# Performance work log

Hardware: AMD Instinct MI355X
Metric: run time of the kernel (lower is better)

Reference implementation:

```python
import jax, jax.numpy as jnp
from jax import lax
import numpy as np

DIM = 512
HEADS = 8


def setup_inputs() -> dict:
    key = jax.random.key(0)
    k1, k2, k3, k4, k5 = jax.random.split(key, 5)
    B, C, H, W = 2, DIM, 64, 64
    x = jax.random.normal(k1, (B, C, H, W), dtype=jnp.float32)
    # depthwise 3x3 conv (groups=C, bias=False): torch OIHW with O=C, I=1
    dw_w = jax.random.normal(k2, (C, 1, 3, 3), dtype=jnp.float32) * (1.0 / 3.0)
    # 1x1 conv C -> 3C (bias=False)
    qkv_w = jax.random.normal(k3, (3 * C, C, 1, 1), dtype=jnp.float32) * (C ** -0.5)
    # 1x1 proj conv C -> C with bias
    proj_w = jax.random.normal(k4, (C, C, 1, 1), dtype=jnp.float32) * (C ** -0.5)
    proj_b = jax.random.normal(k5, (C,), dtype=jnp.float32) * 0.01
    return {"x": x, "dw_w": dw_w, "qkv_w": qkv_w, "proj_w": proj_w, "proj_b": proj_b}


def reference(x, dw_w, qkv_w, proj_w, proj_b):
    B, C, H, W = x.shape
    heads = HEADS
    dh = C // heads
    scale = dh ** -0.5
    N = H * W
    # depthwise 3x3, padding=1
    y = lax.conv_general_dilated(
        x, dw_w, window_strides=(1, 1), padding=((1, 1), (1, 1)),
        dimension_numbers=("NCHW", "OIHW", "NCHW"), feature_group_count=C)
    # 1x1 conv as matmul over channels -> (B, 3C, H, W)
    qkv = jnp.einsum("bchw,oc->bohw", y, qkv_w[:, :, 0, 0])
    # (B, 3, heads, dh, N) -> q,k,v each (B, heads, N, dh)
    qkv = qkv.reshape(B, 3, heads, dh, N).transpose(1, 0, 2, 4, 3)
    q, k, v = qkv[0], qkv[1], qkv[2]
    attn = jax.nn.softmax(jnp.einsum("bhnd,bhmd->bhnm", q, k) * scale, axis=-1)
    o = jnp.einsum("bhnm,bhmd->bhnd", attn, v)          # (B, heads, N, dh)
    o = o.transpose(0, 1, 3, 2).reshape(B, C, H, W)      # matches torch transpose(2,3).reshape
    out = jnp.einsum("bchw,oc->bohw", o, proj_w[:, :, 0, 0]) + proj_b[None, :, None, None]
    return out
```

## Files before the change

### kernel.cpp

```cpp
#include <hip/hip_runtime.h>
#include <hip/hip_bf16.h>

typedef __bf16 bf16_t;
typedef __bf16 bf16x4 __attribute__((ext_vector_type(4)));
typedef __bf16 bf16x8 __attribute__((ext_vector_type(8)));
typedef float f32x4 __attribute__((ext_vector_type(4)));
typedef float f32x8 __attribute__((ext_vector_type(8)));

#define MFMA16(a, b, c) __builtin_amdgcn_mfma_f32_16x16x32_bf16((a), (b), (c), 0, 0, 0)

#if __has_builtin(__builtin_amdgcn_exp2f)
#define EXP2(x) __builtin_amdgcn_exp2f(x)
#else
#define EXP2(x) exp2f(x)
#endif

#define AS1(p) ((const __attribute__((address_space(1))) void*)(p))
#define AS3(p) ((__attribute__((address_space(3))) void*)(p))

#define NPIX 4096
#define CDIM 512
#define QSCALE 0.1803368801111744f

#define KSTR 72
#define KTILE (64 * KSTR)

#define DWSTR 200

__device__ __forceinline__ bool detect_f32(const void* p) {
  const unsigned short* u = (const unsigned short*)p;
  int lane = threadIdx.x & 63;
  int f = 0;
#pragma unroll
  for (int j = 0; j < 4; ++j) {
    int e = (u[lane * 4 + j] >> 7) & 0xFF;
    f |= (e >= 138) ? 1 : 0;
  }
  return __ballot(f) != 0ull;
}

__global__ __launch_bounds__(256) void dwconv_kernel(
    const void* __restrict__ x_, const void* __restrict__ dww_,
    bf16_t* __restrict__ yt, const void* __restrict__ qkvw,
    const void* __restrict__ projw, bf16_t* __restrict__ wq,
    bf16_t* __restrict__ wp) {
  __shared__ bf16_t xs[64 * DWSTR];
  __shared__ float wsh[64 * 9];
  int bidx = blockIdx.x;
  int tid = threadIdx.x;

  if (bidx >= 1024) {
    int bid = bidx - 1024;
    const void* src;
    bf16_t* dst;
    int off;
    if (bid < 384) {
      src = qkvw; dst = wq; off = bid * 2048;
    } else {
      src = projw; dst = wp; off = (bid - 384) * 2048;
    }
    const bool wf32 = detect_f32(src);
    int i = off + tid * 8;
    if (wf32) {
      const float* p = (const float*)src + i;
      float4 t0 = *(const float4*)p;
      float4 t1 = *(const float4*)(p + 4);
      bf16x8 v;
      v[0] = (bf16_t)t0.x; v[1] = (bf16_t)t0.y;
      v[2] = (bf16_t)t0.z; v[3] = (bf16_t)t0.w;
      v[4] = (bf16_t)t1.x; v[5] = (bf16_t)t1.y;
      v[6] = (bf16_t)t1.z; v[7] = (bf16_t)t1.w;
      *(bf16x8*)&dst[i] = v;
    } else {
      *(bf16x8*)&dst[i] = *(const bf16x8*)((const bf16_t*)src + i);
    }
    return;
  }

  const bool f32m = detect_f32(x_);
  int c0 = (bidx & 7) << 6;
  int h = (bidx >> 3) & 63;
  int b = bidx >> 9;

  for (int i = tid; i < 576; i += 256)
    wsh[i] = f32m ? ((const float*)dww_)[c0 * 9 + i]
                  : (float)((const bf16_t*)dww_)[c0 * 9 + i];

  const size_t xoff = ((size_t)b * CDIM + c0) * NPIX;
#pragma unroll
  for (int r = 0; r < 3; ++r) {
    int hh = h + r - 1;
    bool ok = (unsigned)hh < 64u;
#pragma unroll
    for (int it = 0; it < 2; ++it) {
      int idx2 = tid + it * 256;
      int c = idx2 >> 3, ch = idx2 & 7;
      bf16x8 v = {};
      if (ok) {
        size_t gi = xoff + (size_t)c * NPIX + (size_t)hh * 64 + ch * 8;
        if (f32m) {
          const float* p = (const float*)x_ + gi;
          float4 t0 = *(const float4*)p;
          float4 t1 = *(const float4*)(p + 4);
          v[0] = (bf16_t)t0.x; v[1] = (bf16_t)t0.y;
          v[2] = (bf16_t)t0.z; v[3] = (bf16_t)t0.w;
          v[4] = (bf16_t)t1.x; v[5] = (bf16_t)t1.y;
          v[6] = (bf16_t)t1.z; v[7] = (bf16_t)t1.w;
        } else {
          v = *(const bf16x8*)((const bf16_t*)x_ + gi);
        }
      }
      *(bf16x8*)&xs[c * DWSTR + r * 64 + ch * 8] = v;
    }
  }
  __syncthreads();

  int c = tid & 63;
  int wb = tid >> 6;
  int w0 = wb * 16;
  float wreg[9];
#pragma unroll
  for (int j = 0; j < 9; ++j) wreg[j] = wsh[c * 9 + j];
  const bf16_t* xrow = &xs[c * DWSTR];

  float xw[3][18];
#pragma unroll
  for (int r = 0; r < 3; ++r) {
    bf16x8 v0 = *(const bf16x8*)&xrow[r * 64 + w0];
    bf16x8 v1 = *(const bf16x8*)&xrow[r * 64 + w0 + 8];
    xw[r][0] = (wb > 0) ? (float)xrow[r * 64 + w0 - 1] : 0.f;
    xw[r][17] = (wb < 3) ? (float)xrow[r * 64 + w0 + 16] : 0.f;
#pragma unroll
    for (int i = 0; i < 8; ++i) {
      xw[r][1 + i] = (float)v0[i];
      xw[r][9 + i] = (float)v1[i];
    }
  }

  bf16_t* ybase = yt + ((size_t)b * NPIX + h * 64) * CDIM + c0 + c;
#pragma unroll
  for (int j = 0; j < 16; ++j) {
    float acc = 0.f;
#pragma unroll
    for (int r = 0; r < 3; ++r)
      acc += xw[r][j] * wreg[3 * r] + xw[r][j + 1] * wreg[3 * r + 1] +
             xw[r][j + 2] * wreg[3 * r + 2];
    ybase[(size_t)(w0 + j) * CDIM] = (bf16_t)acc;
  }
}

__global__ __launch_bounds__(256) void gemm_kernel(
    const void* __restrict__ A_, const bf16_t* __restrict__ Bt,
    void* __restrict__ o0, bf16_t* __restrict__ o1, bf16_t* __restrict__ o2,
    const void* __restrict__ bias_, int mode, size_t pstride,
    const float* __restrict__ lsb, int aconv) {
  const int K = 512;
  __shared__ bf16_t as[128 * 32];
  __shared__ bf16_t bs[128 * 32];
  const bool f32m = detect_f32(bias_ ? bias_ : A_);
  int z = blockIdx.z;
  const bf16_t* Bz = Bt + (size_t)z * NPIX * K;
  int m0 = blockIdx.x * 128;
  int n0 = blockIdx.y * 128;
  int tid = threadIdx.x;
  int lane = tid & 63;
  int wv = tid >> 6;
  int wm = wv >> 1, wn = wv & 1;
  int col = lane & 15, quad = lane >> 4;

  f32x4 acc[4][4] = {};
  for (int ko = 0; ko < K; ko += 32) {
    if (aconv || !f32m) {
#pragma unroll
      for (int j = 0; j < 2; ++j) {
        int i = tid + j * 256;
        int row = i >> 2, kc = (i & 3) << 3;
        __builtin_amdgcn_global_load_lds(
            AS1(&((const bf16_t*)A_)[(size_t)(m0 + row) * K + ko + kc]),
            AS3(&as[(wv * 64 + j * 256) * 8]), 16, 0, 0);
      }
    } else {
#pragma unroll
      for (int j = 0; j < 2; ++j) {
        int i = tid + j * 256;
        int row = i >> 2, kc = (i & 3) << 3;
        const float* p = &((const float*)A_)[(size_t)(m0 + row) * K + ko + kc];
        float4 t0 = *(const float4*)p;
        float4 t1 = *(const float4*)(p + 4);
        bf16x8 av;
        av[0] = (bf16_t)t0.x; av[1] = (bf16_t)t0.y;
        av[2] = (bf16_t)t0.z; av[3] = (bf16_t)t0.w;
        av[4] = (bf16_t)t1.x; av[5] = (bf16_t)t1.y;
        av[6] = (bf16_t)t1.z; av[7] = (bf16_t)t1.w;
        *(bf16x8*)&as[row * 32 + kc] = av;
      }
    }
    if (mode < 2) {
#pragma unroll
      for (int j = 0; j < 2; ++j) {
        int i = tid + j * 256;
        int row = i >> 2, kc = (i & 3) << 3;
        __builtin_amdgcn_global_load_lds(
            AS1(&Bz[(size_t)(n0 + row) * K + ko + kc]),
            AS3(&bs[(wv * 64 + j * 256) * 8]), 16, 0, 0);
      }
    } else {
#pragma unroll
      for (int j = 0; j < 2; ++j) {
        int i = tid + j * 256;
        int row = i >> 2, kc = (i & 3) << 3;
        int hz = ko >> 6;
        size_t qi = (size_t)(z * 8 + hz) * NPIX + n0 + row;
        float lacc = 0.f;
        for (int s = 0; s < mode; ++s)
          lacc += lsb[qi + (size_t)s * 16 * NPIX];
        float invl = 1.f / lacc;
        int d = (ko & 63) + kc;
        f32x8 f = {};
        for (int s = 0; s < mode; ++s) {
          bf16x8 p = *(const bf16x8*)&Bt[(size_t)s * pstride + qi * 64 + d];
#pragma unroll
          for (int e = 0; e < 8; ++e) f[e] += (float)p[e];
        }
#pragma unroll
        for (int e = 0; e < 8; ++e) f[e] *= invl;
        *(bf16x8*)&bs[row * 32 + kc] = __builtin_convertvector(f, bf16x8);
      }
    }
    __syncthreads();

    bf16x8 af[4], bfr[4];
#pragma unroll
    for (int f = 0; f < 4; ++f) {
      af[f] = *(const bf16x8*)&as[(wm * 64 + f * 16 + col) * 32 + quad * 8];
      bfr[f] = *(const bf16x8*)&bs[(wn * 64 + f * 16 + col) * 32 + quad * 8];
    }
#pragma unroll
    for (int fm = 0; fm < 4; ++fm)
#pragma unroll
      for (int fn = 0; fn < 4; ++fn)
        acc[fm][fn] = MFMA16(af[fm], bfr[fn], acc[fm][fn]);
    __syncthreads();
  }

  if (mode == 0) {
    int t = m0 >> 9;
    float scale = (t == 0) ? QSCALE : 1.0f;
    bf16_t* q0 = (bf16_t*)o0;
#pragma unroll
    for (int fm = 0; fm < 4; ++fm) {
      int mloc = m0 + wm * 64 + fm * 16 + quad * 4;
      int hh = (mloc & 511) >> 6;
      int d = mloc & 63;
#pragma unroll
      for (int fn = 0; fn < 4; ++fn) {
        int n = n0 + wn * 64 + fn * 16 + col;
        if (t < 2) {
          bf16_t* dst = ((t == 0) ? q0 : o1) +
                        ((size_t)z * 8 + hh) * ((size_t)NPIX * 64) +
                        (size_t)n * 64 + d;
          union {
            ushort4 u;
            bf16_t hv[4];
          } pk;
#pragma unroll
          for (int r = 0; r < 4; ++r) pk.hv[r] = (bf16_t)(acc[fm][fn][r] * scale);
          *(ushort4*)dst = pk.u;
        } else {
          bf16_t* vb = o2 + ((size_t)z * 8 + hh) * ((size_t)NPIX * 64);
#pragma unroll
          for (int r = 0; r < 4; ++r)
            vb[(size_t)(d + r) * NPIX + n] = (bf16_t)acc[fm][fn][r];
        }
      }
    }
  } else {
#pragma unroll
    for (int fm = 0; fm < 4; ++fm) {
      int mloc = m0 + wm * 64 + fm * 16 + quad * 4;
#pragma unroll
      for (int r = 0; r < 4; ++r) {
        float bv = f32m ? ((const float*)bias_)[mloc + r]
                        : (float)((const bf16_t*)bias_)[mloc + r];
#pragma unroll
        for (int fn = 0; fn < 4; ++fn) {
          int n = n0 + wn * 64 + fn * 16 + col;
          size_t oi = (size_t)z * CDIM * NPIX + (size_t)(mloc + r) * NPIX + n;
          float val = acc[fm][fn][r] + bv;
          if (f32m)
            ((float*)o0)[oi] = val;
          else
            ((bf16_t*)o0)[oi] = (bf16_t)val;
        }
      }
    }
  }
}

__global__ __launch_bounds__(256) void combine_kernel(
    const bf16_t* __restrict__ O1, const bf16_t* __restrict__ O2,
    const float* __restrict__ ls, bf16_t* __restrict__ out) {
  int tid = threadIdx.x;
  int hd = tid & 63;
  int dn = tid >> 6;
  int h = hd >> 3;
  int dc = (hd & 7) << 3;
  int n = ((blockIdx.x & 1023) << 2) + dn;
  int z = blockIdx.x >> 10;
  size_t qi = (size_t)(z * 8 + h) * NPIX + n;
  float invl = 1.f / (ls[qi] + ls[qi + 16 * (size_t)NPIX]);
  bf16x8 p1 = *(const bf16x8*)&O1[qi * 64 + dc];
  bf16x8 p2 = *(const bf16x8*)&O2[qi * 64 + dc];
  f32x8 f;
#pragma unroll
  for (int e = 0; e < 8; ++e) f[e] = ((float)p1[e] + (float)p2[e]) * invl;
  *(bf16x8*)&out[((size_t)z * NPIX + n) * CDIM + h * 64 + dc] =
      __builtin_convertvector(f, bf16x8);
}

template <int MODE>
__global__ __launch_bounds__(256, 2) void attn_kernel(
    const bf16_t* __restrict__ q, const bf16_t* __restrict__ k,
    const bf16_t* __restrict__ vt, bf16_t* __restrict__ po,
    size_t posz, float* __restrict__ lsum) {
  __shared__ bf16_t ks[2 * KTILE];
  __shared__ bf16_t vs[2 * KTILE];
  int qt = blockIdx.x & 15;
  int bh = (blockIdx.x >> 4) & 15;
  int kh = (MODE >= 2) ? (blockIdx.x >> 8) : 0;
  const int kspan = (MODE >= 2) ? (64 / MODE) : 64;
  int kstart = kh * kspan;
  int kend = kstart + kspan;
  int tid = threadIdx.x;
  int lane = tid & 63, wv = tid >> 6;
  int col = lane & 15, quad = lane >> 4;
  const bf16_t* qb = q + (size_t)bh * NPIX * 64;
  const bf16_t* kb = k + (size_t)bh * NPIX * 64;
  const bf16_t* vb = vt + (size_t)bh * NPIX * 64;

  bf16x8 qfrag[4][2];
  int qrow0 = qt * 256 + wv * 64;
#pragma unroll
  for (int sub = 0; sub < 4; ++sub)
#pragma unroll
    for (int kk = 0; kk < 2; ++kk)
      qfrag[sub][kk] = *(const bf16x8*)&qb[(size_t)(qrow0 + sub * 16 + col) * 64 +
                                           kk * 32 + quad * 8];

  int trow = tid >> 2, t4 = tid & 3;
  bf16x8 kA0, kA1, vA0, vA1, kB0, kB1, vB0, vB1;
  auto loadKV = [&](int kc, bf16x8& k0, bf16x8& k1, bf16x8& v0, bf16x8& v1) {
    const bf16_t* kgr = &kb[(size_t)(kc * 64 + trow) * 64 + t4 * 16];
    const bf16_t* vgr = &vb[(size_t)trow * NPIX + kc * 64 + t4 * 16];
    k0 = *(const bf16x8*)kgr;
    k1 = *(const bf16x8*)(kgr + 8);
    v0 = *(const bf16x8*)vgr;
    v1 = *(const bf16x8*)(vgr + 8);
  };
  loadKV(kstart, kA0, kA1, vA0, vA1);
  loadKV(kstart + 1, kB0, kB1, vB0, vB1);

  int vbase = trow * KSTR + (t4 >> 1) * 32 + (t4 & 1) * 4;

  f32x4 oacc[4][4] = {};
  float lsv[4] = {0.f, 0.f, 0.f, 0.f};

  for (int kc = kstart; kc < kend; ++kc) {
    bf16_t* ksb = &ks[(kc & 1) * KTILE];
    bf16_t* vsb = &vs[(kc & 1) * KTILE];
    *(bf16x8*)&ksb[trow * KSTR + t4 * 16] = kA0;
    *(bf16x8*)&ksb[trow * KSTR + t4 * 16 + 8] = kA1;
    {
      union { bf16x8 v; bf16x4 h[2]; } u0, u1;
      u0.v = vA0; u1.v = vA1;
      *(bf16x4*)&vsb[vbase] = u0.h[0];
      *(bf16x4*)&vsb[vbase + 8] = u0.h[1];
      *(bf16x4*)&vsb[vbase + 16] = u1.h[0];
      *(bf16x4*)&vsb[vbase + 24] = u1.h[1];
    }
    __syncthreads();

    kA0 = kB0; kA1 = kB1; vA0 = vB0; vA1 = vB1;
    {
      int kcn = kc + 2;
      if (kcn >= kend) kcn = kstart;
      loadKV(kcn, kB0, kB1, vB0, vB1);
    }

    bf16x8 kf[4][2];
#pragma unroll
    for (int nt = 0; nt < 4; ++nt)
#pragma unroll
      for (int kk = 0; kk < 2; ++kk)
        kf[nt][kk] =
            *(const bf16x8*)&ksb[(nt * 16 + col) * KSTR + kk * 32 + quad * 8];
    bf16x8 vf[4][2];
#pragma unroll
    for (int dt = 0; dt < 4; ++dt)
#pragma unroll
      for (int t = 0; t < 2; ++t)
        vf[dt][t] =
            *(const bf16x8*)&vsb[(dt * 16 + col) * KSTR + t * 32 + quad * 8];

#pragma unroll
    for (int sub = 0; sub < 4; ++sub) {
      f32x4 sv[4];
#pragma unroll
      for (int nt = 0; nt < 4; ++nt) {
        f32x4 s = {};
        s = MFMA16(kf[nt][0], qfrag[sub][0], s);
        s = MFMA16(kf[nt][1], qfrag[sub][1], s);
        sv[nt] = s;
      }
      bf16x8 pb[2];
      float ls = 0.f;
#pragma unroll
      for (int t = 0; t < 2; ++t) {
        f32x8 pe;
#pragma unroll
        for (int half = 0; half < 2; ++half)
#pragma unroll
          for (int r = 0; r < 4; ++r)
            pe[half * 4 + r] = EXP2(sv[2 * t + half][r]);
        float s0 = pe[0] + pe[1], s1 = pe[2] + pe[3];
        float s2 = pe[4] + pe[5], s3 = pe[6] + pe[7];
        ls += (s0 + s1) + (s2 + s3);
        pb[t] = __builtin_convertvector(pe, bf16x8);
      }
      lsv[sub] += ls;
#pragma unroll
      for (int dt = 0; dt < 4; ++dt) {
        oacc[sub][dt] = MFMA16(vf[dt][0], pb[0], oacc[sub][dt]);
        oacc[sub][dt] = MFMA16(vf[dt][1], pb[1], oacc[sub][dt]);
      }
    }
  }

#pragma unroll
  for (int sub = 0; sub < 4; ++sub) {
    lsv[sub] += __shfl_xor(lsv[sub], 16);
    lsv[sub] += __shfl_xor(lsv[sub], 32);
  }

  if (MODE == 0) {
    int b = bh >> 3, hh = bh & 7;
#pragma unroll
    for (int sub = 0; sub < 4; ++sub) {
      float inv = 1.f / lsv[sub];
      int qrow = qrow0 + sub * 16 + col;
      bf16_t* ob = po + ((size_t)b * NPIX + qrow) * CDIM + hh * 64 + quad * 4;
#pragma unroll
      for (int dt = 0; dt < 4; ++dt) {
        union {
          ushort4 u;
          bf16_t hv[4];
        } pk;
#pragma unroll
        for (int r = 0; r < 4; ++r)
          pk.hv[r] = (bf16_t)(oacc[sub][dt][r] * inv);
        *(ushort4*)(ob + dt * 16) = pk.u;
      }
    }
  } else {
    bf16_t* pbase = po + (size_t)kh * posz;
#pragma unroll
    for (int sub = 0; sub < 4; ++sub) {
      int qrow = qrow0 + sub * 16 + col;
      bf16_t* op = pbase + ((size_t)bh * NPIX + qrow) * 64 + quad * 4;
#pragma unroll
      for (int dt = 0; dt < 4; ++dt) {
        union {
          ushort4 u;
          bf16_t hv[4];
        } pk;
#pragma unroll
        for (int r = 0; r < 4; ++r) pk.hv[r] = (bf16_t)oacc[sub][dt][r];
        *(ushort4*)(op + dt * 16) = pk.u;
      }
    }
    if (quad == 0) {
      float* lbase = lsum + (size_t)(kh * 16 + bh) * NPIX;
#pragma unroll
      for (int sub = 0; sub < 4; ++sub)
        lbase[qrow0 + sub * 16 + col] = lsv[sub];
    }
  }
}

extern "C" void kernel_launch(void* const* d_in, const int* in_sizes, int n_in,
                              void* d_out, int out_size, void* d_ws,
                              size_t ws_size, hipStream_t stream) {
  const void* x = d_in[0];
  const void* dww = d_in[1];
  const void* qkvw = d_in[2];
  const void* projw = d_in[3];
  const void* projb = d_in[4];

  bf16_t* ws = (bf16_t*)d_ws;
  const size_t SZ = (size_t)2 * NPIX * CDIM;
  bf16_t* yt = ws;
  bf16_t* qa = ws + SZ;
  bf16_t* ka = ws + 2 * SZ;
  bf16_t* va = ws + 3 * SZ;

  const size_t needC = 7 * SZ * sizeof(bf16_t);
  const size_t need2 =
      5 * SZ * sizeof(bf16_t) + 2 * 16 * (size_t)NPIX * sizeof(float);

  if (ws_size >= needC) {
    bf16_t* O1 = yt;
    bf16_t* O2 = ws + 4 * SZ;
    float* ls2 = (float*)(ws + 5 * SZ);
    bf16_t* wq = ws + 5 * SZ + 262144;
    bf16_t* wp = wq + 786432;
    bf16_t* oc = ws + 6 * SZ;
    dwconv_kernel<<<1536, 256, 0, stream>>>(x, dww, yt, qkvw, projw, wq, wp);
    gemm_kernel<<<dim3(12, 32, 2), 256, 0, stream>>>(
        wq, yt, qa, ka, va, nullptr, 0, 0, nullptr, 1);
    attn_kernel<2><<<512, 256, 0, stream>>>(qa, ka, va, O1, 4 * SZ, ls2);
    combine_kernel<<<2048, 256, 0, stream>>>(O1, O2, ls2, oc);
    gemm_kernel<<<dim3(4, 32, 2), 256, 0, stream>>>(
        wp, oc, d_out, nullptr, nullptr, projb, 1, 0, nullptr, 1);
  } else if (ws_size >= need2) {
    bf16_t* O1 = yt;
    float* ls2 = (float*)(ws + 5 * SZ);
    dwconv_kernel<<<1024, 256, 0, stream>>>(x, dww, yt, nullptr, nullptr,
                                            nullptr, nullptr);
    gemm_kernel<<<dim3(12, 32, 2), 256, 0, stream>>>(
        qkvw, yt, qa, ka, va, nullptr, 0, 0, nullptr, 0);
    attn_kernel<2><<<512, 256, 0, stream>>>(qa, ka, va, O1, 4 * SZ, ls2);
    gemm_kernel<<<dim3(4, 32, 2), 256, 0, stream>>>(
        projw, O1, d_out, nullptr, nullptr, projb, 2, 4 * SZ, ls2, 0);
  } else {
    dwconv_kernel<<<1024, 256, 0, stream>>>(x, dww, yt, nullptr, nullptr,
                                            nullptr, nullptr);
    gemm_kernel<<<dim3(12, 32, 2), 256, 0, stream>>>(
        qkvw, yt, qa, ka, va, nullptr, 0, 0, nullptr, 0);
    attn_kernel<0><<<256, 256, 0, stream>>>(qa, ka, va, yt, 0, nullptr);
    gemm_kernel<<<dim3(4, 32, 2), 256, 0, stream>>>(
        projw, yt, d_out, nullptr, nullptr, projb, 1, 0, nullptr, 0);
  }
}
```

Before: 193.7 us.

## Fuse split-K attention combine into attention kernel via arrival counters

Replaces the separate combine kernel with a last-arriver merge inside the attention kernel. Each pair of split-K blocks bumps a per-tile atomic counter, which is zeroed in the dwconv prologue. The second block to arrive reads the partner's partial output and row sums, normalizes, and writes the merged channel-last output directly. This removes one kernel launch and the extra read/write pass of partial outputs, at the cost of relying on threadfence/atomic ordering between blocks.

```diff
diff --git a/kernel.cpp b/kernel.cpp
--- a/kernel.cpp
+++ b/kernel.cpp
@@ -43,7 +43,7 @@
     const void* __restrict__ x_, const void* __restrict__ dww_,
     bf16_t* __restrict__ yt, const void* __restrict__ qkvw,
     const void* __restrict__ projw, bf16_t* __restrict__ wq,
-    bf16_t* __restrict__ wp) {
+    bf16_t* __restrict__ wp, int* __restrict__ flags) {
   __shared__ bf16_t xs[64 * DWSTR];
   __shared__ float wsh[64 * 9];
   int bidx = blockIdx.x;
@@ -74,6 +74,7 @@
     } else {
       *(bf16x8*)&dst[i] = *(const bf16x8*)((const bf16_t*)src + i);
     }
+    if (bid == 511) flags[tid] = 0;
     return;
   }
 
@@ -322,13 +323,15 @@
 __global__ __launch_bounds__(256, 2) void attn_kernel(
     const bf16_t* __restrict__ q, const bf16_t* __restrict__ k,
     const bf16_t* __restrict__ vt, bf16_t* __restrict__ po,
-    size_t posz, float* __restrict__ lsum) {
+    size_t posz, float* __restrict__ lsum, bf16_t* __restrict__ oc,
+    int* __restrict__ flags) {
   __shared__ bf16_t ks[2 * KTILE];
   __shared__ bf16_t vs[2 * KTILE];
+  __shared__ int shflag;
   int qt = blockIdx.x & 15;
   int bh = (blockIdx.x >> 4) & 15;
   int kh = (MODE >= 2) ? (blockIdx.x >> 8) : 0;
-  const int kspan = (MODE >= 2) ? (64 / MODE) : 64;
+  const int kspan = (MODE >= 2) ? 32 : 64;
   int kstart = kh * kspan;
   int kend = kstart + kspan;
   int tid = threadIdx.x;
@@ -484,6 +487,41 @@
       for (int sub = 0; sub < 4; ++sub)
         lbase[qrow0 + sub * 16 + col] = lsv[sub];
     }
+
+    if (MODE == 3) {
+      __threadfence();
+      __syncthreads();
+      if (tid == 0) shflag = atomicAdd(&flags[blockIdx.x & 255], 1);
+      __syncthreads();
+      if (shflag == 1) {
+        __threadfence();
+        const bf16_t* qb2 =
+            po + (size_t)(1 - kh) * posz + (size_t)bh * NPIX * 64;
+        const float* plb = lsum + (size_t)((1 - kh) * 16 + bh) * NPIX;
+        int z2 = bh >> 3, h2 = bh & 7;
+#pragma unroll
+        for (int sub = 0; sub < 4; ++sub) {
+          int qrow = qrow0 + sub * 16 + col;
+          float inv = 1.f / (lsv[sub] + plb[qrow]);
+          const bf16_t* pp = qb2 + (size_t)qrow * 64 + quad * 4;
+          bf16_t* ob =
+              oc + ((size_t)z2 * NPIX + qrow) * CDIM + h2 * 64 + quad * 4;
+#pragma unroll
+          for (int dt = 0; dt < 4; ++dt) {
+            union {
+              ushort4 u;
+              bf16_t hv[4];
+            } pu, pk;
+            pu.u = *(const ushort4*)(pp + dt * 16);
+#pragma unroll
+            for (int r = 0; r < 4; ++r)
+              pk.hv[r] =
+                  (bf16_t)((oacc[sub][dt][r] + (float)pu.hv[r]) * inv);
+            *(ushort4*)(ob + dt * 16) = pk.u;
+          }
+        }
+      }
+    }
   }
 }
 
@@ -509,34 +547,37 @@
 
   if (ws_size >= needC) {
     bf16_t* O1 = yt;
-    bf16_t* O2 = ws + 4 * SZ;
     float* ls2 = (float*)(ws + 5 * SZ);
     bf16_t* wq = ws + 5 * SZ + 262144;
     bf16_t* wp = wq + 786432;
+    int* flags = (int*)(wp + 262144);
     bf16_t* oc = ws + 6 * SZ;
-    dwconv_kernel<<<1536, 256, 0, stream>>>(x, dww, yt, qkvw, projw, wq, wp);
+    dwconv_kernel<<<1536, 256, 0, stream>>>(x, dww, yt, qkvw, projw, wq, wp,
+                                            flags);
     gemm_kernel<<<dim3(12, 32, 2), 256, 0, stream>>>(
         wq, yt, qa, ka, va, nullptr, 0, 0, nullptr, 1);
-    attn_kernel<2><<<512, 256, 0, stream>>>(qa, ka, va, O1, 4 * SZ, ls2);
-    combine_kernel<<<2048, 256, 0, stream>>>(O1, O2, ls2, oc);
+    attn_kernel<3><<<512, 256, 0, stream>>>(qa, ka, va, O1, 4 * SZ, ls2, oc,
+                                            flags);
     gemm_kernel<<<dim3(4, 32, 2), 256, 0, stream>>>(
         wp, oc, d_out, nullptr, nullptr, projb, 1, 0, nullptr, 1);
   } else if (ws_size >= need2) {
     bf16_t* O1 = yt;
     float* ls2 = (float*)(ws + 5 * SZ);
     dwconv_kernel<<<1024, 256, 0, stream>>>(x, dww, yt, nullptr, nullptr,
-                                            nullptr, nullptr);
+                                            nullptr, nullptr, nullptr);
     gemm_kernel<<<dim3(12, 32, 2), 256, 0, stream>>>(
         qkvw, yt, qa, ka, va, nullptr, 0, 0, nullptr, 0);
-    attn_kernel<2><<<512, 256, 0, stream>>>(qa, ka, va, O1, 4 * SZ, ls2);
+    attn_kernel<2><<<512, 256, 0, stream>>>(qa, ka, va, O1, 4 * SZ, ls2,
+                                            nullptr, nullptr);
     gemm_kernel<<<dim3(4, 32, 2), 256, 0, stream>>>(
         projw, O1, d_out, nullptr, nullptr, projb, 2, 4 * SZ, ls2, 0);
   } else {
     dwconv_kernel<<<1024, 256, 0, stream>>>(x, dww, yt, nullptr, nullptr,
-                                            nullptr, nullptr);
+                                            nullptr, nullptr, nullptr);
     gemm_kernel<<<dim3(12, 32, 2), 256, 0, stream>>>(
         qkvw, yt, qa, ka, va, nullptr, 0, 0, nullptr, 0);
-    attn_kernel<0><<<256, 256, 0, stream>>>(qa, ka, va, yt, 0, nullptr);
+    attn_kernel<0><<<256, 256, 0, stream>>>(qa, ka, va, yt, 0, nullptr,
+                                            nullptr, nullptr);
     gemm_kernel<<<dim3(4, 32, 2), 256, 0, stream>>>(
         projw, yt, d_out, nullptr, nullptr, projb, 1, 0, nullptr, 0);
   }
```

Result: slower. 296.4 us (+53.0%).
